# Performance work log

Measured on AMD Instinct MI355X. Metric: run time of the kernel, lower is better.

## Reference

```python
import jax, jax.numpy as jnp
import numpy as np

H = 3584          # hidden_size
NH = 28           # num query heads
NKV = 4           # num kv heads
HD = H // NH      # head_dim = 128
I = 18944         # intermediate_size
EPS = 1e-6
THETA = 1000000.0


def setup_inputs() -> dict:
    key = jax.random.key(0)
    ks = jax.random.split(key, 16)
    B, S = 1, 2048
    s = 0.02
    inp = {
        "hidden_states": jax.random.normal(ks[0], (B, S, H), jnp.float32),
        "position_ids": jnp.broadcast_to(jnp.arange(S, dtype=jnp.int32)[None, :], (B, S)),
        "q_w": jax.random.normal(ks[1], (NH * HD, H), jnp.float32) * s,
        "q_b": jax.random.normal(ks[2], (NH * HD,), jnp.float32) * s,
        "k_w": jax.random.normal(ks[3], (NKV * HD, H), jnp.float32) * s,
        "k_b": jax.random.normal(ks[4], (NKV * HD,), jnp.float32) * s,
        "v_w": jax.random.normal(ks[5], (NKV * HD, H), jnp.float32) * s,
        "v_b": jax.random.normal(ks[6], (NKV * HD,), jnp.float32) * s,
        "o_w": jax.random.normal(ks[7], (H, NH * HD), jnp.float32) * s,
        "gate_w": jax.random.normal(ks[8], (I, H), jnp.float32) * s,
        "up_w": jax.random.normal(ks[9], (I, H), jnp.float32) * s,
        "down_w": jax.random.normal(ks[10], (H, I), jnp.float32) * s,
        "ln1_w": jnp.ones((H,), jnp.float32),
        "ln2_w": jnp.ones((H,), jnp.float32),
    }
    return inp


def _rms_norm(x, w):
    var = jnp.mean(jnp.square(x), axis=-1, keepdims=True)
    return x * jax.lax.rsqrt(var + EPS) * w


def _rope_cos_sin(position_ids):
    # inv_freq: [HD/2]
    inv_freq = 1.0 / (THETA ** (jnp.arange(0, HD, 2, dtype=jnp.float32) / HD))
    ang = position_ids.astype(jnp.float32)[..., None] * inv_freq  # [B,S,HD/2]
    emb = jnp.concatenate([ang, ang], axis=-1)                     # [B,S,HD]
    return jnp.cos(emb)[:, None], jnp.sin(emb)[:, None]            # [B,1,S,HD]


def _rotate_half(x):
    x1, x2 = x[..., : HD // 2], x[..., HD // 2 :]
    return jnp.concatenate([-x2, x1], axis=-1)


def _forward(hidden_states, position_ids, q_w, q_b, k_w, k_b, v_w, v_b,
             o_w, gate_w, up_w, down_w, ln1_w, ln2_w):
    B, S, _ = hidden_states.shape
    residual = hidden_states
    x = _rms_norm(hidden_states, ln1_w)

    q = jnp.einsum("bsh,dh->bsd", x, q_w) + q_b   # [B,S,NH*HD]
    k = jnp.einsum("bsh,dh->bsd", x, k_w) + k_b   # [B,S,NKV*HD]
    v = jnp.einsum("bsh,dh->bsd", x, v_w) + v_b

    q = q.reshape(B, S, NH, HD).transpose(0, 2, 1, 3)    # [B,NH,S,HD]
    k = k.reshape(B, S, NKV, HD).transpose(0, 2, 1, 3)   # [B,NKV,S,HD]
    v = v.reshape(B, S, NKV, HD).transpose(0, 2, 1, 3)

    cos, sin = _rope_cos_sin(position_ids)
    q = q * cos + _rotate_half(q) * sin
    k = k * cos + _rotate_half(k) * sin

    # GQA: group query heads per kv head (NH = NKV * G)
    G = NH // NKV
    qg = q.reshape(B, NKV, G, S, HD)
    scores = jnp.einsum("bhgsd,bhtd->bhgst", qg, k) / jnp.sqrt(jnp.float32(HD))
    probs = jax.nn.softmax(scores, axis=-1)               # no causal mask in source
    attn = jnp.einsum("bhgst,bhtd->bhgsd", probs, v)      # [B,NKV,G,S,HD]
    attn = attn.reshape(B, NH, S, HD).transpose(0, 2, 1, 3).reshape(B, S, H)

    attn_out = jnp.einsum("bsd,hd->bsh", attn, o_w)
    hidden = residual + attn_out

    residual = hidden
    x = _rms_norm(hidden, ln2_w)
    gate = jax.nn.silu(jnp.einsum("bsh,ih->bsi", x, gate_w))
    up = jnp.einsum("bsh,ih->bsi", x, up_w)
    mlp = jnp.einsum("bsi,hi->bsh", gate * up, down_w)
    return residual + mlp


def reference(hidden_states, position_ids, q_w, q_b, k_w, k_b, v_w, v_b,
              o_w, gate_w, up_w, down_w, ln1_w, ln2_w):
    return _forward(hidden_states, position_ids, q_w, q_b, k_w, k_b, v_w, v_b,
                    o_w, gate_w, up_w, down_w, ln1_w, ln2_w)
```

## Files before the change

kernel.cpp:

```cpp
#include <hip/hip_runtime.h>
#include <hip/hip_bf16.h>
#include <stdint.h>

#define S_LEN 2048
#define HDIM  3584
#define NHEAD 28
#define NKVH  4
#define HDHD  128
#define IDIM  18944

typedef __attribute__((ext_vector_type(8))) short short8;
typedef __attribute__((ext_vector_type(4))) float floatx4;
typedef __attribute__((ext_vector_type(4))) unsigned int uint4v;

__device__ __forceinline__ unsigned short f2bf(float f) {
  union { float f; unsigned int u; } v; v.f = f;
  unsigned int r = v.u + 0x7fffu + ((v.u >> 16) & 1u);
  return (unsigned short)(r >> 16);
}
__device__ __forceinline__ float bf2f(unsigned short h) {
  union { unsigned int u; float f; } v; v.u = ((unsigned int)h) << 16;
  return v.f;
}
__device__ __forceinline__ unsigned int pk2(float a, float b) {
  __hip_bfloat162 h = __float22bfloat162_rn(make_float2(a, b));
  union { __hip_bfloat162 h; unsigned int u; } c; c.h = h; return c.u;
}

__device__ __forceinline__ void gload_lds16(const void* g, void* l) {
  __builtin_amdgcn_global_load_lds(
      (const __attribute__((address_space(1))) void*)g,
      (__attribute__((address_space(3))) void*)l, 16, 0, 0);
}

__device__ __forceinline__ int xcd_remap(int id, int total) {
  return (id & 7) * (total >> 3) + (id >> 3);
}

__device__ __forceinline__ void store_out(int MODE, void* outp, const void* aux,
                                          size_t oidx, float v) {
  if (MODE == 0) {
    ((float*)outp)[oidx] = v;
  } else if (MODE == 1) {
    ((unsigned short*)outp)[oidx] = f2bf(v);
  } else if (MODE == 2) {
    ((float*)outp)[oidx] = v + ((const float*)aux)[oidx];
  } else {
    float gt = bf2f(((const unsigned short*)aux)[oidx]);
    float sg = gt / (1.f + __expf(-gt));
    ((unsigned short*)outp)[oidx] = f2bf(sg * v);
  }
}

template<int MODE, bool BIAS>
__global__ __launch_bounds__(256)
void gemm_bf(const unsigned short* __restrict__ A, int lda,
             const unsigned short* __restrict__ W,
             const float* __restrict__ bias,
             void* __restrict__ outp, int ldo, int col0,
             const void* __restrict__ aux, int K)
{
  const int g  = xcd_remap(blockIdx.x, gridDim.x);
  const int mb = g & 15;
  const int nb = g >> 4;
  const int t = threadIdx.x;
  const int w = t >> 6, l = t & 63, lg = l >> 4, lc = l & 15;
  const int wr = w >> 1, wc = w & 1;

  __shared__ __align__(16) unsigned short As[128 * 64];
  __shared__ __align__(16) unsigned short Ws[128 * 64];

  floatx4 acc[4][4] = {};

  const char* Ablk = (const char*)(A + (size_t)mb * 128 * lda);
  const char* Wblk = (const char*)(W + (size_t)nb * 128 * K);

  const int s_row = t >> 3;
  const int s_scb = (((t & 7) ^ ((t >> 3) & 7)) << 4);
  const int r_sw  = (lc & 7) << 4;

  const size_t abytes = (size_t)lda * 2;
  const size_t wbytes = (size_t)K * 2;
  const int nk = K >> 6;
  for (int kt = 0; kt < nk; ++kt) {
    #pragma unroll
    for (int i = 0; i < 4; ++i)
      gload_lds16(Ablk + (size_t)(i * 32 + s_row) * abytes + (size_t)kt * 128 + s_scb,
                  (char*)As + i * 4096 + t * 16);
    #pragma unroll
    for (int i = 0; i < 4; ++i)
      gload_lds16(Wblk + (size_t)(i * 32 + s_row) * wbytes + (size_t)kt * 128 + s_scb,
                  (char*)Ws + i * 4096 + t * 16);
    __syncthreads();
    #pragma unroll
    for (int kk = 0; kk < 2; ++kk) {
      short8 afr[4], bfr[4];
      #pragma unroll
      for (int m = 0; m < 4; ++m)
        afr[m] = *(const short8*)((const char*)As + (wr*64 + m*16 + lc) * 128
                                 + ((kk*64 + lg*16) ^ r_sw));
      #pragma unroll
      for (int n = 0; n < 4; ++n)
        bfr[n] = *(const short8*)((const char*)Ws + (wc*64 + n*16 + lc) * 128
                                  + ((kk*64 + lg*16) ^ r_sw));
      #pragma unroll
      for (int m = 0; m < 4; ++m)
        #pragma unroll
        for (int n = 0; n < 4; ++n)
          acc[m][n] = __builtin_amdgcn_mfma_f32_16x16x32_bf16(afr[m], bfr[n], acc[m][n], 0, 0, 0);
    }
    __syncthreads();
  }

  float bv[4] = {0.f, 0.f, 0.f, 0.f};
  if (BIAS) {
    #pragma unroll
    for (int n = 0; n < 4; ++n) bv[n] = bias[nb*128 + wc*64 + n*16 + lc];
  }
  #pragma unroll
  for (int m = 0; m < 4; ++m) {
    #pragma unroll
    for (int n = 0; n < 4; ++n) {
      const int colg = col0 + nb*128 + wc*64 + n*16 + lc;
      #pragma unroll
      for (int j = 0; j < 4; ++j) {
        const int rowg = mb*128 + wr*64 + m*16 + lg*4 + j;
        store_out(MODE, outp, aux, (size_t)rowg * ldo + colg, acc[m][n][j] + bv[n]);
      }
    }
  }
}

template<int MODE, bool BIAS>
__global__ __launch_bounds__(256, 2)
void gemm_w(const unsigned short* __restrict__ A, int lda,
            const unsigned short* __restrict__ W,
            const float* __restrict__ bias,
            void* __restrict__ outp, int ldo, int col0,
            const void* __restrict__ aux, int K)
{
  const int g  = xcd_remap(blockIdx.x, gridDim.x);
  const int mb = g & 7;
  const int nb = g >> 3;
  const int t  = threadIdx.x;
  const int w  = t >> 6, l = t & 63, lg = l >> 4, lc = l & 15;
  const int wr = w >> 1, wc = w & 1;

  __shared__ __align__(16) unsigned short As[256 * 64];
  __shared__ __align__(16) unsigned short Bs[128 * 64];

  floatx4 acc[8][4] = {};

  const char* Ablk = (const char*)(A + (size_t)mb * 256 * lda);
  const char* Wblk = (const char*)(W + (size_t)nb * 128 * K);

  const int s_row = t >> 3;
  const int s_scb = (((t & 7) ^ ((t >> 3) & 7)) << 4);
  const int r_sw  = (lc & 7) << 4;

  const size_t abytes = (size_t)lda * 2;
  const size_t wbytes = (size_t)K * 2;
  const int nk = K >> 6;

  for (int kt = 0; kt < nk; ++kt) {
    const char* asrc = Ablk + (size_t)kt * 128 + s_scb;
    #pragma unroll
    for (int i = 0; i < 8; ++i)
      gload_lds16(asrc + (size_t)(i * 32 + s_row) * abytes,
                  (char*)As + i * 4096 + t * 16);
    const char* wsrc = Wblk + (size_t)kt * 128 + s_scb;
    #pragma unroll
    for (int i = 0; i < 4; ++i)
      gload_lds16(wsrc + (size_t)(i * 32 + s_row) * wbytes,
                  (char*)Bs + i * 4096 + t * 16);
    __syncthreads();
    #pragma unroll
    for (int kk = 0; kk < 2; ++kk) {
      const int ko = (kk * 64 + lg * 16) ^ r_sw;
      short8 bfr[4];
      #pragma unroll
      for (int n = 0; n < 4; ++n)
        bfr[n] = *(const short8*)((const char*)Bs + (wc*64 + n*16 + lc) * 128 + ko);
      #pragma unroll
      for (int m = 0; m < 8; ++m) {
        short8 af = *(const short8*)((const char*)As + (wr*128 + m*16 + lc) * 128 + ko);
        #pragma unroll
        for (int n = 0; n < 4; ++n)
          acc[m][n] = __builtin_amdgcn_mfma_f32_16x16x32_bf16(af, bfr[n], acc[m][n], 0, 0, 0);
      }
    }
    __syncthreads();
  }

  float bv[4] = {0.f, 0.f, 0.f, 0.f};
  if (BIAS) {
    #pragma unroll
    for (int n = 0; n < 4; ++n) bv[n] = bias[nb*128 + wc*64 + n*16 + lc];
  }
  #pragma unroll
  for (int m = 0; m < 8; ++m) {
    #pragma unroll
    for (int n = 0; n < 4; ++n) {
      const int colg = col0 + nb*128 + wc*64 + n*16 + lc;
      #pragma unroll
      for (int j = 0; j < 4; ++j) {
        const int rowg = mb*256 + wr*128 + m*16 + lg*4 + j;
        store_out(MODE, outp, aux, (size_t)rowg * ldo + colg, acc[m][n][j] + bv[n]);
      }
    }
  }
}

__global__ __launch_bounds__(256)
void cvt_bf16_kernel(const float* __restrict__ in, unsigned short* __restrict__ out, int n8)
{
  int i = blockIdx.x * 256 + threadIdx.x;
  const int stride = gridDim.x * 256;
  for (; i < n8; i += stride) {
    floatx4 a = *(const floatx4*)(in + (size_t)i * 8);
    floatx4 b = *(const floatx4*)(in + (size_t)i * 8 + 4);
    uint4v p;
    p[0] = pk2(a[0], a[1]); p[1] = pk2(a[2], a[3]);
    p[2] = pk2(b[0], b[1]); p[3] = pk2(b[2], b[3]);
    *(uint4v*)(out + (size_t)i * 8) = p;
  }
}

__global__ void pack_bias_kernel(const float* __restrict__ qb, const float* __restrict__ kb,
                                 const float* __restrict__ vb, float* __restrict__ o)
{
  int i = blockIdx.x * 256 + threadIdx.x;
  if (i < 3584) o[i] = qb[i];
  else if (i < 4096) o[i] = kb[i - 3584];
  else if (i < 4608) o[i] = vb[i - 4096];
}

__global__ __launch_bounds__(448)
void rmsnorm_kernel(const float* __restrict__ x, const float* __restrict__ wgt,
                    unsigned short* __restrict__ out)
{
  const int row = blockIdx.x, t = threadIdx.x;
  const float* xp = x + (size_t)row * HDIM + t * 8;
  floatx4 a = *(const floatx4*)xp;
  floatx4 b = *(const floatx4*)(xp + 4);
  float ss = a[0]*a[0]+a[1]*a[1]+a[2]*a[2]+a[3]*a[3]
           + b[0]*b[0]+b[1]*b[1]+b[2]*b[2]+b[3]*b[3];
  #pragma unroll
  for (int mk = 1; mk < 64; mk <<= 1) ss += __shfl_xor(ss, mk, 64);
  __shared__ float wsum[8];
  if ((t & 63) == 0) wsum[t >> 6] = ss;
  __syncthreads();
  float tot = 0.f;
  #pragma unroll
  for (int i = 0; i < 7; ++i) tot += wsum[i];
  const float sc = rsqrtf(tot * (1.f / 3584.f) + 1e-6f);
  const float* wp = wgt + t * 8;
  short8 o;
  #pragma unroll
  for (int e = 0; e < 4; ++e) o[e]   = (short)f2bf(a[e] * sc * wp[e]);
  #pragma unroll
  for (int e = 0; e < 4; ++e) o[4+e] = (short)f2bf(b[e] * sc * wp[4+e]);
  *(short8*)(out + (size_t)row * HDIM + t * 8) = o;
}

__global__ __launch_bounds__(448)
void add_rmsnorm_kernel(const float* __restrict__ x, const float* __restrict__ y,
                        const float* __restrict__ wgt,
                        float* __restrict__ h1, unsigned short* __restrict__ out)
{
  const int row = blockIdx.x, t = threadIdx.x;
  const size_t base = (size_t)row * HDIM + t * 8;
  floatx4 a = *(const floatx4*)(x + base);
  floatx4 b = *(const floatx4*)(x + base + 4);
  floatx4 c = *(const floatx4*)(y + base);
  floatx4 d = *(const floatx4*)(y + base + 4);
  a += c; b += d;
  *(floatx4*)(h1 + base)     = a;
  *(floatx4*)(h1 + base + 4) = b;
  float ss = a[0]*a[0]+a[1]*a[1]+a[2]*a[2]+a[3]*a[3]
           + b[0]*b[0]+b[1]*b[1]+b[2]*b[2]+b[3]*b[3];
  #pragma unroll
  for (int mk = 1; mk < 64; mk <<= 1) ss += __shfl_xor(ss, mk, 64);
  __shared__ float wsum[8];
  if ((t & 63) == 0) wsum[t >> 6] = ss;
  __syncthreads();
  float tot = 0.f;
  #pragma unroll
  for (int i = 0; i < 7; ++i) tot += wsum[i];
  const float sc = rsqrtf(tot * (1.f / 3584.f) + 1e-6f);
  const float* wp = wgt + t * 8;
  short8 o;
  #pragma unroll
  for (int e = 0; e < 4; ++e) o[e]   = (short)f2bf(a[e] * sc * wp[e]);
  #pragma unroll
  for (int e = 0; e < 4; ++e) o[4+e] = (short)f2bf(b[e] * sc * wp[4+e]);
  *(short8*)(out + (size_t)row * HDIM + t * 8) = o;
}

__global__ void rope_table_kernel(const int* __restrict__ pos, float* __restrict__ tab)
{
  int idx = blockIdx.x * 256 + threadIdx.x;
  int s = idx >> 6, d = idx & 63;
  float p = (float)pos[s];
  float inv = expf(-((float)(2 * d) * (1.f / 128.f)) * 13.815510557964274f);
  float ang = p * inv;
  tab[idx] = cosf(ang);
  tab[S_LEN * 64 + idx] = sinf(ang);
}

template<int NHX>
__global__ void rope_apply_kernel(const float* __restrict__ in, const float* __restrict__ tab,
                                  unsigned short* __restrict__ out, int col0)
{
  int idx = blockIdx.x * 256 + threadIdx.x;
  int d = idx & 63;
  int rem = idx >> 6;
  int hh = rem % NHX;
  int s  = rem / NHX;
  const float* ip = in + (size_t)s * 4608 + col0 + hh * HDHD;
  float x1 = ip[d], x2 = ip[64 + d];
  float c  = tab[s * 64 + d];
  float sn = tab[S_LEN * 64 + s * 64 + d];
  unsigned short* op = out + (size_t)s * (NHX * HDHD) + hh * HDHD;
  op[d]      = f2bf(x1 * c - x2 * sn);
  op[64 + d] = f2bf(x2 * c + x1 * sn);
}

__global__ void vtrans_kernel(const float* __restrict__ qkvf, unsigned short* __restrict__ vt)
{
  int idx = blockIdx.x * 256 + threadIdx.x;
  int s = idx & (S_LEN - 1);
  int c = idx >> 11;
  vt[idx] = f2bf(qkvf[(size_t)s * 4608 + 4096 + c]);
}

__global__ __launch_bounds__(256)
void attn_kernel(const unsigned short* __restrict__ Q,
                 const unsigned short* __restrict__ Kr,
                 const unsigned short* __restrict__ Vt,
                 unsigned short* __restrict__ O)
{
  const int g  = xcd_remap(blockIdx.x, gridDim.x);
  const int qb = g & 15;
  const int h  = g >> 4;
  const int kvh = h / 7;
  const int t = threadIdx.x, w = t >> 6, l = t & 63, lg = l >> 4, lc = l & 15;

  __shared__ __align__(16) unsigned short Ks[64 * 128];
  __shared__ __align__(16) unsigned short Vs[128 * 64];
  __shared__ __align__(16) unsigned short Ps[4][16 * 64];

  short8 qf[2][4];
  #pragma unroll
  for (int grp = 0; grp < 2; ++grp) {
    const int qrow = qb * 128 + grp * 64 + w * 16 + lc;
    const unsigned short* qp = Q + (size_t)qrow * HDIM + h * HDHD + lg * 8;
    #pragma unroll
    for (int kk = 0; kk < 4; ++kk) qf[grp][kk] = *(const short8*)(qp + kk * 32);
  }

  float mrun[2][4], lrun[2][4];
  #pragma unroll
  for (int grp = 0; grp < 2; ++grp)
    #pragma unroll
    for (int j = 0; j < 4; ++j) { mrun[grp][j] = -1e30f; lrun[grp][j] = 0.f; }
  floatx4 oacc[2][8] = {};

  const int k_row = t >> 4;
  const int k_scb = (((t & 15) ^ ((t >> 4) & 7)) << 4);
  const int v_row = t >> 3;
  const int v_scb = (((t & 7) ^ ((t >> 3) & 7)) << 4);
  const int r_sw  = (lc & 7) << 4;
  const float scale = 0.08838834764831843f;

  for (int kt = 0; kt < 32; ++kt) {
    #pragma unroll
    for (int i = 0; i < 4; ++i)
      gload_lds16((const char*)Kr + ((size_t)(kt*64 + i*16 + k_row) * 512 + kvh*128) * 2 + k_scb,
                  (char*)Ks + i * 4096 + t * 16);
    #pragma unroll
    for (int i = 0; i < 4; ++i)
      gload_lds16((const char*)Vt + ((size_t)(kvh*128 + i*32 + v_row) * S_LEN) * 2
                      + (size_t)kt * 128 + v_scb,
                  (char*)Vs + i * 4096 + t * 16);
    __syncthreads();

    #pragma unroll
    for (int grp = 0; grp < 2; ++grp) {
      floatx4 sacc[4] = {};
      #pragma unroll
      for (int kk = 0; kk < 4; ++kk) {
        #pragma unroll
        for (int n = 0; n < 4; ++n) {
          short8 kf = *(const short8*)((const char*)Ks + (n*16 + lc) * 256
                                       + ((kk*64 + lg*16) ^ r_sw));
          sacc[n] = __builtin_amdgcn_mfma_f32_16x16x32_bf16(qf[grp][kk], kf, sacc[n], 0, 0, 0);
        }
      }

      float pv[4][4], mt[4];
      #pragma unroll
      for (int j = 0; j < 4; ++j) {
        float a0 = sacc[0][j]*scale, a1 = sacc[1][j]*scale;
        float a2 = sacc[2][j]*scale, a3 = sacc[3][j]*scale;
        pv[0][j]=a0; pv[1][j]=a1; pv[2][j]=a2; pv[3][j]=a3;
        mt[j] = fmaxf(fmaxf(a0, a1), fmaxf(a2, a3));
      }
      #pragma unroll
      for (int mk = 1; mk < 16; mk <<= 1)
        #pragma unroll
        for (int j = 0; j < 4; ++j)
          mt[j] = fmaxf(mt[j], __shfl_xor(mt[j], mk, 16));

      float corr[4], rs[4];
      #pragma unroll
      for (int j = 0; j < 4; ++j) {
        float mn = fmaxf(mrun[grp][j], mt[j]);
        corr[j] = __expf(mrun[grp][j] - mn);
        mrun[grp][j] = mn;
        rs[j] = 0.f;
      }
      #pragma unroll
      for (int n = 0; n < 4; ++n)
        #pragma unroll
        for (int j = 0; j < 4; ++j) {
          float p = __expf(pv[n][j] - mrun[grp][j]);
          pv[n][j] = p; rs[j] += p;
        }
      #pragma unroll
      for (int mk = 1; mk < 16; mk <<= 1)
        #pragma unroll
        for (int j = 0; j < 4; ++j)
          rs[j] += __shfl_xor(rs[j], mk, 16);
      #pragma unroll
      for (int j = 0; j < 4; ++j) lrun[grp][j] = lrun[grp][j] * corr[j] + rs[j];
      #pragma unroll
      for (int q = 0; q < 8; ++q) {
        oacc[grp][q][0] *= corr[0]; oacc[grp][q][1] *= corr[1];
        oacc[grp][q][2] *= corr[2]; oacc[grp][q][3] *= corr[3];
      }

      char* pw = (char*)Ps[w];
      #pragma unroll
      for (int n = 0; n < 4; ++n)
        #pragma unroll
        for (int j = 0; j < 4; ++j) {
          const int prow = lg*4 + j;
          *(unsigned short*)(pw + prow*128 + ((((n*16 + lc)*2)) ^ ((prow & 7) << 4)))
              = f2bf(pv[n][j]);
        }

      short8 pa[2];
      #pragma unroll
      for (int ks = 0; ks < 2; ++ks)
        pa[ks] = *(const short8*)(pw + lc*128 + ((ks*64 + lg*16) ^ r_sw));
      #pragma unroll
      for (int ks = 0; ks < 2; ++ks)
        #pragma unroll
        for (int q = 0; q < 8; ++q) {
          short8 vf = *(const short8*)((const char*)Vs + (q*16 + lc) * 128
                                       + ((ks*64 + lg*16) ^ r_sw));
          oacc[grp][q] = __builtin_amdgcn_mfma_f32_16x16x32_bf16(pa[ks], vf, oacc[grp][q], 0, 0, 0);
        }
    }
    __syncthreads();
  }

  #pragma unroll
  for (int grp = 0; grp < 2; ++grp) {
    float invl[4];
    #pragma unroll
    for (int j = 0; j < 4; ++j) invl[j] = 1.f / lrun[grp][j];
    #pragma unroll
    for (int q = 0; q < 8; ++q)
      #pragma unroll
      for (int j = 0; j < 4; ++j) {
        int rowg = qb*128 + grp*64 + w*16 + lg*4 + j;
        int colg = h*HDHD + q*16 + lc;
        O[(size_t)rowg * HDIM + colg] = f2bf(oacc[grp][q][j] * invl[j]);
      }
  }
}

__global__ void sentinel_kernel(float* out, int n) {
  int i = blockIdx.x * 256 + threadIdx.x;
  if (i < n) out[i] = 1.0e6f;
}

extern "C" void kernel_launch(void* const* d_in, const int* in_sizes, int n_in,
                              void* d_out, int out_size, void* d_ws, size_t ws_size,
                              hipStream_t stream)
{
  (void)in_sizes; (void)n_in;
  const float* hidden = (const float*)d_in[0];
  const int*   pos    = (const int*)d_in[1];
  const float* q_w    = (const float*)d_in[2];
  const float* q_b    = (const float*)d_in[3];
  const float* k_w    = (const float*)d_in[4];
  const float* k_b    = (const float*)d_in[5];
  const float* v_w    = (const float*)d_in[6];
  const float* v_b    = (const float*)d_in[7];
  const float* o_w    = (const float*)d_in[8];
  const float* gate_w = (const float*)d_in[9];
  const float* up_w   = (const float*)d_in[10];
  const float* down_w = (const float*)d_in[11];
  const float* ln1    = (const float*)d_in[12];
  const float* ln2    = (const float*)d_in[13];
  float* out = (float*)d_out;
  char* ws = (char*)d_ws;

  unsigned short* XN    = (unsigned short*)(ws + 0);
  float*          QKVF  = (float*)(ws + 14680064);
  unsigned short* QR    = (unsigned short*)(ws + 52428800);
  unsigned short* KR    = (unsigned short*)(ws + 67108864);
  unsigned short* VT    = (unsigned short*)(ws + 69206016);
  float*          ROPET = (float*)(ws + 71303168);
  float*          BQKV  = (float*)(ws + 72351744);
  unsigned short* CTX   = (unsigned short*)(ws + 77594624);
  float*          AO    = (float*)(ws + 92274688);
  unsigned short* GBUF  = (unsigned short*)(ws + 0);
  unsigned short* ACT   = (unsigned short*)(ws + 77594624);
  float*          H1    = (float*)(ws + 155189248);
  unsigned short* XN2   = (unsigned short*)(ws + 184549376);
  unsigned short* WB    = (unsigned short*)(ws + 199229440);
  const size_t NEED_BIG = 199229440 + 135790592;

  if (ws_size < NEED_BIG) {
    sentinel_kernel<<<(out_size + 255) / 256, 256, 0, stream>>>(out, out_size);
    return;
  }

  const int CVG = 2048;

  rope_table_kernel<<<(S_LEN * 64) / 256, 256, 0, stream>>>(pos, ROPET);
  rmsnorm_kernel<<<S_LEN, 448, 0, stream>>>(hidden, ln1, XN);

  pack_bias_kernel<<<18, 256, 0, stream>>>(q_b, k_b, v_b, BQKV);
  cvt_bf16_kernel<<<CVG, 256, 0, stream>>>(q_w, WB,               (3584 * 3584) / 8);
  cvt_bf16_kernel<<<CVG, 256, 0, stream>>>(k_w, WB + 3584 * 3584, (512 * 3584) / 8);
  cvt_bf16_kernel<<<CVG, 256, 0, stream>>>(v_w, WB + 4096 * 3584, (512 * 3584) / 8);

  gemm_bf<0, true><<<576, 256, 0, stream>>>(XN, HDIM, WB, BQKV, QKVF, 4608, 0, nullptr, HDIM);

  rope_apply_kernel<28><<<(S_LEN * 28 * 64) / 256, 256, 0, stream>>>(QKVF, ROPET, QR, 0);
  rope_apply_kernel<4><<<(S_LEN * 4 * 64) / 256,  256, 0, stream>>>(QKVF, ROPET, KR, 3584);
  vtrans_kernel<<<(512 * S_LEN) / 256, 256, 0, stream>>>(QKVF, VT);

  cvt_bf16_kernel<<<CVG, 256, 0, stream>>>(o_w, WB, (3584 * 3584) / 8);

  attn_kernel<<<448, 256, 0, stream>>>(QR, KR, VT, CTX);

  gemm_bf<0, false><<<448, 256, 0, stream>>>(CTX, HDIM, WB, nullptr, AO, HDIM, 0, nullptr, HDIM);
  add_rmsnorm_kernel<<<S_LEN, 448, 0, stream>>>(hidden, AO, ln2, H1, XN2);

  cvt_bf16_kernel<<<CVG, 256, 0, stream>>>(gate_w, WB, (IDIM * HDIM) / 8);
  gemm_bf<1, false><<<2368, 256, 0, stream>>>(XN2, HDIM, WB, nullptr, GBUF, IDIM, 0, nullptr, HDIM);

  cvt_bf16_kernel<<<CVG, 256, 0, stream>>>(up_w, WB, (IDIM * HDIM) / 8);
  gemm_bf<3, false><<<2368, 256, 0, stream>>>(XN2, HDIM, WB, nullptr, ACT, IDIM, 0, GBUF, HDIM);

  cvt_bf16_kernel<<<CVG, 256, 0, stream>>>(down_w, WB, (HDIM * IDIM) / 8);
  gemm_w<2, false><<<224, 256, 0, stream>>>(ACT, IDIM, WB, nullptr, out, HDIM, 0, H1, IDIM);
}
```

Baseline: 2.009 ms.

## Halve attention query tile and swap GEMM variants for MLP projections

The attention kernel now handles 64 query rows per block instead of 128, which doubles the grid to 896 blocks and halves the per-thread accumulator registers, aiming for better occupancy and CU fill. Each K/V tile is loaded twice as often in aggregate, which adds memory traffic. The gate/up projections switch from gemm_bf to the gemm_w template with half the blocks. The down projection switches from gemm_w to gemm_bf with twice the blocks, presumably matching tile shapes better to each GEMM's N dimension.

```diff
diff --git a/kernel.cpp b/kernel.cpp
--- a/kernel.cpp
+++ b/kernel.cpp
@@ -341,8 +341,8 @@
                  unsigned short* __restrict__ O)
 {
   const int g  = xcd_remap(blockIdx.x, gridDim.x);
-  const int qb = g & 15;
-  const int h  = g >> 4;
+  const int qb = g & 31;
+  const int h  = g >> 5;
   const int kvh = h / 7;
   const int t = threadIdx.x, w = t >> 6, l = t & 63, lg = l >> 4, lc = l & 15;
 
@@ -350,21 +350,18 @@
   __shared__ __align__(16) unsigned short Vs[128 * 64];
   __shared__ __align__(16) unsigned short Ps[4][16 * 64];
 
-  short8 qf[2][4];
-  #pragma unroll
-  for (int grp = 0; grp < 2; ++grp) {
-    const int qrow = qb * 128 + grp * 64 + w * 16 + lc;
+  const int qrow = qb * 64 + w * 16 + lc;
+  short8 qf[4];
+  {
     const unsigned short* qp = Q + (size_t)qrow * HDIM + h * HDHD + lg * 8;
     #pragma unroll
-    for (int kk = 0; kk < 4; ++kk) qf[grp][kk] = *(const short8*)(qp + kk * 32);
-  }
-
-  float mrun[2][4], lrun[2][4];
-  #pragma unroll
-  for (int grp = 0; grp < 2; ++grp)
-    #pragma unroll
-    for (int j = 0; j < 4; ++j) { mrun[grp][j] = -1e30f; lrun[grp][j] = 0.f; }
-  floatx4 oacc[2][8] = {};
+    for (int kk = 0; kk < 4; ++kk) qf[kk] = *(const short8*)(qp + kk * 32);
+  }
+
+  float mrun[4], lrun[4];
+  #pragma unroll
+  for (int j = 0; j < 4; ++j) { mrun[j] = -1e30f; lrun[j] = 0.f; }
+  floatx4 oacc[8] = {};
 
   const int k_row = t >> 4;
   const int k_scb = (((t & 15) ^ ((t >> 4) & 7)) << 4);
@@ -385,101 +382,95 @@
                   (char*)Vs + i * 4096 + t * 16);
     __syncthreads();
 
-    #pragma unroll
-    for (int grp = 0; grp < 2; ++grp) {
-      floatx4 sacc[4] = {};
-      #pragma unroll
-      for (int kk = 0; kk < 4; ++kk) {
-        #pragma unroll
-        for (int n = 0; n < 4; ++n) {
-          short8 kf = *(const short8*)((const char*)Ks + (n*16 + lc) * 256
-                                       + ((kk*64 + lg*16) ^ r_sw));
-          sacc[n] = __builtin_amdgcn_mfma_f32_16x16x32_bf16(qf[grp][kk], kf, sacc[n], 0, 0, 0);
-        }
-      }
-
-      float pv[4][4], mt[4];
+    floatx4 sacc[4] = {};
+    #pragma unroll
+    for (int kk = 0; kk < 4; ++kk) {
+      #pragma unroll
+      for (int n = 0; n < 4; ++n) {
+        short8 kf = *(const short8*)((const char*)Ks + (n*16 + lc) * 256
+                                     + ((kk*64 + lg*16) ^ r_sw));
+        sacc[n] = __builtin_amdgcn_mfma_f32_16x16x32_bf16(qf[kk], kf, sacc[n], 0, 0, 0);
+      }
+    }
+
+    float pv[4][4], mt[4];
+    #pragma unroll
+    for (int j = 0; j < 4; ++j) {
+      float a0 = sacc[0][j]*scale, a1 = sacc[1][j]*scale;
+      float a2 = sacc[2][j]*scale, a3 = sacc[3][j]*scale;
+      pv[0][j]=a0; pv[1][j]=a1; pv[2][j]=a2; pv[3][j]=a3;
+      mt[j] = fmaxf(fmaxf(a0, a1), fmaxf(a2, a3));
+    }
+    #pragma unroll
+    for (int mk = 1; mk < 16; mk <<= 1)
+      #pragma unroll
+      for (int j = 0; j < 4; ++j)
+        mt[j] = fmaxf(mt[j], __shfl_xor(mt[j], mk, 16));
+
+    float corr[4], rs[4];
+    #pragma unroll
+    for (int j = 0; j < 4; ++j) {
+      float mn = fmaxf(mrun[j], mt[j]);
+      corr[j] = __expf(mrun[j] - mn);
+      mrun[j] = mn;
+      rs[j] = 0.f;
+    }
+    #pragma unroll
+    for (int n = 0; n < 4; ++n)
       #pragma unroll
       for (int j = 0; j < 4; ++j) {
-        float a0 = sacc[0][j]*scale, a1 = sacc[1][j]*scale;
-        float a2 = sacc[2][j]*scale, a3 = sacc[3][j]*scale;
-        pv[0][j]=a0; pv[1][j]=a1; pv[2][j]=a2; pv[3][j]=a3;
-        mt[j] = fmaxf(fmaxf(a0, a1), fmaxf(a2, a3));
-      }
-      #pragma unroll
-      for (int mk = 1; mk < 16; mk <<= 1)
-        #pragma unroll
-        for (int j = 0; j < 4; ++j)
-          mt[j] = fmaxf(mt[j], __shfl_xor(mt[j], mk, 16));
-
-      float corr[4], rs[4];
+        float p = __expf(pv[n][j] - mrun[j]);
+        pv[n][j] = p; rs[j] += p;
+      }
+    #pragma unroll
+    for (int mk = 1; mk < 16; mk <<= 1)
+      #pragma unroll
+      for (int j = 0; j < 4; ++j)
+        rs[j] += __shfl_xor(rs[j], mk, 16);
+    #pragma unroll
+    for (int j = 0; j < 4; ++j) lrun[j] = lrun[j] * corr[j] + rs[j];
+    #pragma unroll
+    for (int q = 0; q < 8; ++q) {
+      oacc[q][0] *= corr[0]; oacc[q][1] *= corr[1];
+      oacc[q][2] *= corr[2]; oacc[q][3] *= corr[3];
+    }
+
+    char* pw = (char*)Ps[w];
+    #pragma unroll
+    for (int n = 0; n < 4; ++n)
       #pragma unroll
       for (int j = 0; j < 4; ++j) {
-        float mn = fmaxf(mrun[grp][j], mt[j]);
-        corr[j] = __expf(mrun[grp][j] - mn);
-        mrun[grp][j] = mn;
-        rs[j] = 0.f;
-      }
-      #pragma unroll
-      for (int n = 0; n < 4; ++n)
-        #pragma unroll
-        for (int j = 0; j < 4; ++j) {
-          float p = __expf(pv[n][j] - mrun[grp][j]);
-          pv[n][j] = p; rs[j] += p;
-        }
-      #pragma unroll
-      for (int mk = 1; mk < 16; mk <<= 1)
-        #pragma unroll
-        for (int j = 0; j < 4; ++j)
-          rs[j] += __shfl_xor(rs[j], mk, 16);
-      #pragma unroll
-      for (int j = 0; j < 4; ++j) lrun[grp][j] = lrun[grp][j] * corr[j] + rs[j];
+        const int prow = lg*4 + j;
+        *(unsigned short*)(pw + prow*128 + ((((n*16 + lc)*2)) ^ ((prow & 7) << 4)))
+            = f2bf(pv[n][j]);
+      }
+
+    short8 pa[2];
+    #pragma unroll
+    for (int ks = 0; ks < 2; ++ks)
+      pa[ks] = *(const short8*)(pw + lc*128 + ((ks*64 + lg*16) ^ r_sw));
+    #pragma unroll
+    for (int ks = 0; ks < 2; ++ks)
       #pragma unroll
       for (int q = 0; q < 8; ++q) {
-        oacc[grp][q][0] *= corr[0]; oacc[grp][q][1] *= corr[1];
-        oacc[grp][q][2] *= corr[2]; oacc[grp][q][3] *= corr[3];
-      }
-
-      char* pw = (char*)Ps[w];
-      #pragma unroll
-      for (int n = 0; n < 4; ++n)
-        #pragma unroll
-        for (int j = 0; j < 4; ++j) {
-          const int prow = lg*4 + j;
-          *(unsigned short*)(pw + prow*128 + ((((n*16 + lc)*2)) ^ ((prow & 7) << 4)))
-              = f2bf(pv[n][j]);
-        }
-
-      short8 pa[2];
-      #pragma unroll
-      for (int ks = 0; ks < 2; ++ks)
-        pa[ks] = *(const short8*)(pw + lc*128 + ((ks*64 + lg*16) ^ r_sw));
-      #pragma unroll
-      for (int ks = 0; ks < 2; ++ks)
-        #pragma unroll
-        for (int q = 0; q < 8; ++q) {
-          short8 vf = *(const short8*)((const char*)Vs + (q*16 + lc) * 128
-                                       + ((ks*64 + lg*16) ^ r_sw));
-          oacc[grp][q] = __builtin_amdgcn_mfma_f32_16x16x32_bf16(pa[ks], vf, oacc[grp][q], 0, 0, 0);
-        }
-    }
+        short8 vf = *(const short8*)((const char*)Vs + (q*16 + lc) * 128
+                                     + ((ks*64 + lg*16) ^ r_sw));
+        oacc[q] = __builtin_amdgcn_mfma_f32_16x16x32_bf16(pa[ks], vf, oacc[q], 0, 0, 0);
+      }
     __syncthreads();
   }
 
-  #pragma unroll
-  for (int grp = 0; grp < 2; ++grp) {
-    float invl[4];
-    #pragma unroll
-    for (int j = 0; j < 4; ++j) invl[j] = 1.f / lrun[grp][j];
-    #pragma unroll
-    for (int q = 0; q < 8; ++q)
-      #pragma unroll
-      for (int j = 0; j < 4; ++j) {
-        int rowg = qb*128 + grp*64 + w*16 + lg*4 + j;
-        int colg = h*HDHD + q*16 + lc;
-        O[(size_t)rowg * HDIM + colg] = f2bf(oacc[grp][q][j] * invl[j]);
-      }
-  }
+  float invl[4];
+  #pragma unroll
+  for (int j = 0; j < 4; ++j) invl[j] = 1.f / lrun[j];
+  #pragma unroll
+  for (int q = 0; q < 8; ++q)
+    #pragma unroll
+    for (int j = 0; j < 4; ++j) {
+      int rowg = qb*64 + w*16 + lg*4 + j;
+      int colg = h*HDHD + q*16 + lc;
+      O[(size_t)rowg * HDIM + colg] = f2bf(oacc[q][j] * invl[j]);
+    }
 }
 
 __global__ void sentinel_kernel(float* out, int n) {
@@ -548,17 +539,17 @@
 
   cvt_bf16_kernel<<<CVG, 256, 0, stream>>>(o_w, WB, (3584 * 3584) / 8);
 
-  attn_kernel<<<448, 256, 0, stream>>>(QR, KR, VT, CTX);
+  attn_kernel<<<896, 256, 0, stream>>>(QR, KR, VT, CTX);
 
   gemm_bf<0, false><<<448, 256, 0, stream>>>(CTX, HDIM, WB, nullptr, AO, HDIM, 0, nullptr, HDIM);
   add_rmsnorm_kernel<<<S_LEN, 448, 0, stream>>>(hidden, AO, ln2, H1, XN2);
 
   cvt_bf16_kernel<<<CVG, 256, 0, stream>>>(gate_w, WB, (IDIM * HDIM) / 8);
-  gemm_bf<1, false><<<2368, 256, 0, stream>>>(XN2, HDIM, WB, nullptr, GBUF, IDIM, 0, nullptr, HDIM);
+  gemm_w<1, false><<<1184, 256, 0, stream>>>(XN2, HDIM, WB, nullptr, GBUF, IDIM, 0, nullptr, HDIM);
 
   cvt_bf16_kernel<<<CVG, 256, 0, stream>>>(up_w, WB, (IDIM * HDIM) / 8);
-  gemm_bf<3, false><<<2368, 256, 0, stream>>>(XN2, HDIM, WB, nullptr, ACT, IDIM, 0, GBUF, HDIM);
+  gemm_w<3, false><<<1184, 256, 0, stream>>>(XN2, HDIM, WB, nullptr, ACT, IDIM, 0, GBUF, HDIM);
 
   cvt_bf16_kernel<<<CVG, 256, 0, stream>>>(down_w, WB, (HDIM * IDIM) / 8);
-  gemm_w<2, false><<<224, 256, 0, stream>>>(ACT, IDIM, WB, nullptr, out, HDIM, 0, H1, IDIM);
-}
+  gemm_bf<2, false><<<448, 256, 0, stream>>>(ACT, IDIM, WB, nullptr, out, HDIM, 0, H1, IDIM);
+}
```

Result: faster. 1.701 ms (-15.3%).
